# Kernel optimization log

Hardware: AMD Instinct MI355X
Metric: run time of the kernel (lower is better)

## Reference

```python
import jax, jax.numpy as jnp
import numpy as np

EPS = 1e-6


def _rmsnorm(x, weight, eps=EPS):
    # float32 compute, cast back to input dtype, then scale (matches torch module)
    xf = x.astype(jnp.float32)
    rms = jax.lax.rsqrt(jnp.mean(xf * xf, axis=-1, keepdims=True) + eps)
    return (xf * rms).astype(x.dtype) * weight


def _block_attn_res(V, pseudo_query, norm_weight):
    # V: [n, b, t, d]; pseudo_query, norm_weight: [d]
    K = _rmsnorm(V, norm_weight)                          # [n,b,t,d]
    d = pseudo_query.shape[-1]
    logits = jnp.einsum('d,nbtd->nbt', pseudo_query, K) / jnp.sqrt(jnp.float32(d))
    attn = jax.nn.softmax(logits, axis=0)                 # softmax over block axis n
    return jnp.einsum('nbt,nbtd->btd', attn, V)           # [b,t,d]


def setup_inputs() -> dict:
    key = jax.random.key(0)
    ks = jax.random.split(key, 4)
    N, B, T, D = 7, 2, 4096, 2048
    return {
        'blocks': jax.random.normal(ks[0], (N, B, T, D), dtype=jnp.float32),
        'partial_block': jax.random.normal(ks[1], (B, T, D), dtype=jnp.float32),
        'pseudo_query_attn': jax.random.normal(ks[2], (D,), dtype=jnp.float32),
        'pseudo_query_mlp': jax.random.normal(ks[3], (D,), dtype=jnp.float32),
        'norm_weight_attn': jnp.ones((D,), dtype=jnp.float32),
        'norm_weight_mlp': jnp.ones((D,), dtype=jnp.float32),
    }


def reference(blocks, partial_block, pseudo_query_attn, pseudo_query_mlp,
              norm_weight_attn, norm_weight_mlp):
    # V = stack(blocks + [partial_block], dim=0): [N+1, B, T, D]
    V = jnp.concatenate([blocks, partial_block[None]], axis=0)
    h_attn = _block_attn_res(V, pseudo_query_attn, norm_weight_attn)
    h_mlp = _block_attn_res(V, pseudo_query_mlp, norm_weight_mlp)
    return (h_attn, h_mlp)
```

## Files before the change

kernel.cpp:

```cpp
#include <hip/hip_runtime.h>

#define NB 8
#define DDIM 2048
#define THREADS 256
#define PER 8

typedef float f32x4 __attribute__((ext_vector_type(4)));

__device__ __forceinline__ float wave_sum64(float x) {
    int t;
    t = __builtin_amdgcn_update_dpp(0, __float_as_int(x), 0x111, 0xf, 0xf, false);
    x += __int_as_float(t);
    t = __builtin_amdgcn_update_dpp(0, __float_as_int(x), 0x112, 0xf, 0xf, false);
    x += __int_as_float(t);
    t = __builtin_amdgcn_update_dpp(0, __float_as_int(x), 0x114, 0xf, 0xf, false);
    x += __int_as_float(t);
    t = __builtin_amdgcn_update_dpp(0, __float_as_int(x), 0x118, 0xf, 0xf, false);
    x += __int_as_float(t);
    t = __builtin_amdgcn_update_dpp(0, __float_as_int(x), 0x142, 0xa, 0xf, false);
    x += __int_as_float(t);
    t = __builtin_amdgcn_update_dpp(0, __float_as_int(x), 0x143, 0xc, 0xf, false);
    x += __int_as_float(t);
    return x;
}

__global__ __launch_bounds__(THREADS, 4)
void block_attn_res_kernel(
    const float* __restrict__ blocks,
    const float* __restrict__ partial,
    const float* __restrict__ qa,
    const float* __restrict__ qm,
    const float* __restrict__ wa,
    const float* __restrict__ wm,
    float* __restrict__ out,
    int BT)
{
    const int row = blockIdx.x;
    const int tid = threadIdx.x;
    const int d0  = tid * PER;

    const size_t rowOff  = (size_t)row * DDIM + d0;
    const size_t nStride = (size_t)BT * DDIM;

    f32x4 qwa[2], qwm[2];
#pragma unroll
    for (int k = 0; k < 2; ++k) {
        const f32x4 q4a = *reinterpret_cast<const f32x4*>(qa + d0 + 4 * k);
        const f32x4 w4a = *reinterpret_cast<const f32x4*>(wa + d0 + 4 * k);
        const f32x4 q4m = *reinterpret_cast<const f32x4*>(qm + d0 + 4 * k);
        const f32x4 w4m = *reinterpret_cast<const f32x4*>(wm + d0 + 4 * k);
        qwa[k] = q4a * w4a;
        qwm[k] = q4m * w4m;
    }

    f32x4 v[NB][2];
    float ss[NB], da[NB], dm[NB];

#pragma unroll
    for (int n = 0; n < NB; ++n) {
        const float* src = (n < NB - 1) ? (blocks + (size_t)n * nStride + rowOff)
                                        : (partial + rowOff);
        v[n][0] = *reinterpret_cast<const f32x4*>(src);
        v[n][1] = *reinterpret_cast<const f32x4*>(src + 4);
        float s = 0.f, pa = 0.f, pm = 0.f;
#pragma unroll
        for (int k = 0; k < 2; ++k) {
#pragma unroll
            for (int j = 0; j < 4; ++j) {
                s  += v[n][k][j] * v[n][k][j];
                pa += qwa[k][j]  * v[n][k][j];
                pm += qwm[k][j]  * v[n][k][j];
            }
        }
        ss[n] = s; da[n] = pa; dm[n] = pm;
    }

#pragma unroll
    for (int n = 0; n < NB; ++n) {
        ss[n] = wave_sum64(ss[n]);
        da[n] = wave_sum64(da[n]);
        dm[n] = wave_sum64(dm[n]);
    }

    __shared__ float red[4 * 24];
    const int wave = tid >> 6;
    if ((tid & 63) == 63) {
#pragma unroll
        for (int n = 0; n < NB; ++n) {
            red[wave * 24 + n]      = ss[n];
            red[wave * 24 + 8 + n]  = da[n];
            red[wave * 24 + 16 + n] = dm[n];
        }
    }
    __syncthreads();

    float tot[24];
    {
        const f32x4* r4 = reinterpret_cast<const f32x4*>(red);
#pragma unroll
        for (int g = 0; g < 6; ++g) {
            f32x4 a = r4[g], b = r4[6 + g], c = r4[12 + g], d = r4[18 + g];
            f32x4 s4 = a + b + c + d;
            tot[4 * g + 0] = s4.x;
            tot[4 * g + 1] = s4.y;
            tot[4 * g + 2] = s4.z;
            tot[4 * g + 3] = s4.w;
        }
    }

    float aw[NB], mw[NB];
    {
        const float inv_sqrt_d = rsqrtf((float)DDIM);
        float lga[NB], lgm[NB];
#pragma unroll
        for (int n = 0; n < NB; ++n) {
            float rms = rsqrtf(tot[n] * (1.0f / DDIM) + 1e-6f);
            lga[n] = tot[8 + n]  * rms * inv_sqrt_d;
            lgm[n] = tot[16 + n] * rms * inv_sqrt_d;
        }
        float ma = lga[0], mm = lgm[0];
#pragma unroll
        for (int n = 1; n < NB; ++n) { ma = fmaxf(ma, lga[n]); mm = fmaxf(mm, lgm[n]); }
        float sa = 0.f, sm = 0.f;
#pragma unroll
        for (int n = 0; n < NB; ++n) {
            aw[n] = __expf(lga[n] - ma); sa += aw[n];
            mw[n] = __expf(lgm[n] - mm); sm += mw[n];
        }
        const float ra = 1.f / sa, rm = 1.f / sm;
#pragma unroll
        for (int n = 0; n < NB; ++n) { aw[n] *= ra; mw[n] *= rm; }
    }

    f32x4 oa[2], om[2];
#pragma unroll
    for (int k = 0; k < 2; ++k) {
        oa[k] = (f32x4)(0.f);
        om[k] = (f32x4)(0.f);
    }
#pragma unroll
    for (int n = 0; n < NB; ++n) {
#pragma unroll
        for (int k = 0; k < 2; ++k) {
            oa[k] += aw[n] * v[n][k];
            om[k] += mw[n] * v[n][k];
        }
    }

    float* outa = out + rowOff;
    float* outm = out + nStride + rowOff;
    *reinterpret_cast<f32x4*>(outa)     = oa[0];
    *reinterpret_cast<f32x4*>(outa + 4) = oa[1];
    *reinterpret_cast<f32x4*>(outm)     = om[0];
    *reinterpret_cast<f32x4*>(outm + 4) = om[1];
}

extern "C" void kernel_launch(void* const* d_in, const int* in_sizes, int n_in,
                              void* d_out, int out_size, void* d_ws, size_t ws_size,
                              hipStream_t stream)
{
    const float* blocks  = (const float*)d_in[0];
    const float* partial = (const float*)d_in[1];
    const float* qa      = (const float*)d_in[2];
    const float* qm      = (const float*)d_in[3];
    const float* wa      = (const float*)d_in[4];
    const float* wm      = (const float*)d_in[5];
    float* out = (float*)d_out;

    const int D  = in_sizes[2];
    const int BT = in_sizes[1] / D;

    dim3 grid(BT), block(THREADS);
    hipLaunchKernelGGL(block_attn_res_kernel, grid, block, 0, stream,
                       blocks, partial, qa, qm, wa, wm, out, BT);
}
```

Measured before the change: 133.4 us.

## Use persistent blocks with double-buffered row prefetch across rows

The kernel now launches a fixed grid of 512 blocks of 512 threads instead of one block per row. Each block loops over its strided rows and prefetches the next row's eight block vectors into registers while the current row is reduced and written. The goal is to hide global load latency and cut block launch overhead in this memory-bound kernel. The cost is extra registers for two row buffers, two shared-memory barriers per row, and a hardcoded assumption that the row count divides evenly by the grid size.

New measurement: 176.9 us. +32.6%, slower.

```diff
diff --git a/kernel.cpp b/kernel.cpp
--- a/kernel.cpp
+++ b/kernel.cpp
@@ -2,8 +2,9 @@
 
 #define NB 8
 #define DDIM 2048
-#define THREADS 256
-#define PER 8
+#define THREADS 512
+#define NBLK 512
+#define NWAVES (THREADS / 64)
 
 typedef float f32x4 __attribute__((ext_vector_type(4)));
 
@@ -24,6 +25,11 @@
     return x;
 }
 
+__device__ __forceinline__ void barrier_lgkm() {
+    asm volatile("s_waitcnt lgkmcnt(0)" ::: "memory");
+    __builtin_amdgcn_s_barrier();
+}
+
 __global__ __launch_bounds__(THREADS, 4)
 void block_attn_res_kernel(
     const float* __restrict__ blocks,
@@ -35,124 +41,120 @@
     float* __restrict__ out,
     int BT)
 {
-    const int row = blockIdx.x;
     const int tid = threadIdx.x;
-    const int d0  = tid * PER;
+    const int b   = blockIdx.x;
+    const int c   = tid * 4;
+    const size_t nStride = (size_t)BT * DDIM;
+    const int rpb = BT / NBLK;
 
-    const size_t rowOff  = (size_t)row * DDIM + d0;
-    const size_t nStride = (size_t)BT * DDIM;
+    __shared__ float red[2][NWAVES * 24];
+    __shared__ float totl[2][24];
 
-    f32x4 qwa[2], qwm[2];
+    const f32x4 qwa = *reinterpret_cast<const f32x4*>(qa + c) *
+                      *reinterpret_cast<const f32x4*>(wa + c);
+    const f32x4 qwm = *reinterpret_cast<const f32x4*>(qm + c) *
+                      *reinterpret_cast<const f32x4*>(wm + c);
+
+    f32x4 vA[NB], vB[NB];
+
+    auto rowbase = [&](int i) -> size_t {
+        return (size_t)(i * NBLK + b) * DDIM + c;
+    };
+    auto load_row = [&](f32x4* v, size_t rb) {
 #pragma unroll
-    for (int k = 0; k < 2; ++k) {
-        const f32x4 q4a = *reinterpret_cast<const f32x4*>(qa + d0 + 4 * k);
-        const f32x4 w4a = *reinterpret_cast<const f32x4*>(wa + d0 + 4 * k);
-        const f32x4 q4m = *reinterpret_cast<const f32x4*>(qm + d0 + 4 * k);
-        const f32x4 w4m = *reinterpret_cast<const f32x4*>(wm + d0 + 4 * k);
-        qwa[k] = q4a * w4a;
-        qwm[k] = q4m * w4m;
-    }
+        for (int n = 0; n < NB; ++n) {
+            const float* src = (n < NB - 1) ? (blocks + (size_t)n * nStride + rb)
+                                            : (partial + rb);
+            v[n] = *reinterpret_cast<const f32x4*>(src);
+        }
+    };
 
-    f32x4 v[NB][2];
-    float ss[NB], da[NB], dm[NB];
-
+    auto process = [&](const f32x4* v, float* redb, float* totb, size_t rb) {
+        float ss[NB], da[NB], dm[NB];
 #pragma unroll
-    for (int n = 0; n < NB; ++n) {
-        const float* src = (n < NB - 1) ? (blocks + (size_t)n * nStride + rowOff)
-                                        : (partial + rowOff);
-        v[n][0] = *reinterpret_cast<const f32x4*>(src);
-        v[n][1] = *reinterpret_cast<const f32x4*>(src + 4);
-        float s = 0.f, pa = 0.f, pm = 0.f;
-#pragma unroll
-        for (int k = 0; k < 2; ++k) {
+        for (int n = 0; n < NB; ++n) {
+            float s = 0.f, pa = 0.f, pm = 0.f;
 #pragma unroll
             for (int j = 0; j < 4; ++j) {
-                s  += v[n][k][j] * v[n][k][j];
-                pa += qwa[k][j]  * v[n][k][j];
-                pm += qwm[k][j]  * v[n][k][j];
+                s  += v[n][j] * v[n][j];
+                pa += qwa[j]  * v[n][j];
+                pm += qwm[j]  * v[n][j];
+            }
+            ss[n] = wave_sum64(s);
+            da[n] = wave_sum64(pa);
+            dm[n] = wave_sum64(pm);
+        }
+        const int wave = tid >> 6;
+        if ((tid & 63) == 63) {
+#pragma unroll
+            for (int n = 0; n < NB; ++n) {
+                redb[wave * 24 + n]      = ss[n];
+                redb[wave * 24 + 8 + n]  = da[n];
+                redb[wave * 24 + 16 + n] = dm[n];
             }
         }
-        ss[n] = s; da[n] = pa; dm[n] = pm;
-    }
+        barrier_lgkm();
+        if (tid < 24) {
+            float s = 0.f;
+#pragma unroll
+            for (int w = 0; w < NWAVES; ++w) s += redb[w * 24 + tid];
+            totb[tid] = s;
+        }
+        barrier_lgkm();
 
+        float t24[24];
+        {
+            const f32x4* t4 = reinterpret_cast<const f32x4*>(totb);
 #pragma unroll
-    for (int n = 0; n < NB; ++n) {
-        ss[n] = wave_sum64(ss[n]);
-        da[n] = wave_sum64(da[n]);
-        dm[n] = wave_sum64(dm[n]);
-    }
+            for (int g = 0; g < 6; ++g) {
+                f32x4 x = t4[g];
+                t24[4 * g + 0] = x.x; t24[4 * g + 1] = x.y;
+                t24[4 * g + 2] = x.z; t24[4 * g + 3] = x.w;
+            }
+        }
 
-    __shared__ float red[4 * 24];
-    const int wave = tid >> 6;
-    if ((tid & 63) == 63) {
+        float aw[NB], mw[NB];
+        {
+            const float inv_sqrt_d = rsqrtf((float)DDIM);
+            float lga[NB], lgm[NB];
+#pragma unroll
+            for (int n = 0; n < NB; ++n) {
+                float rms = rsqrtf(t24[n] * (1.0f / DDIM) + 1e-6f);
+                lga[n] = t24[8 + n]  * rms * inv_sqrt_d;
+                lgm[n] = t24[16 + n] * rms * inv_sqrt_d;
+            }
+            float ma = lga[0], mm = lgm[0];
+#pragma unroll
+            for (int n = 1; n < NB; ++n) { ma = fmaxf(ma, lga[n]); mm = fmaxf(mm, lgm[n]); }
+            float sa = 0.f, sm = 0.f;
+#pragma unroll
+            for (int n = 0; n < NB; ++n) {
+                aw[n] = __expf(lga[n] - ma); sa += aw[n];
+                mw[n] = __expf(lgm[n] - mm); sm += mw[n];
+            }
+            const float ra = 1.f / sa, rm = 1.f / sm;
+#pragma unroll
+            for (int n = 0; n < NB; ++n) { aw[n] *= ra; mw[n] *= rm; }
+        }
+
+        f32x4 oa = (f32x4)(0.f), om = (f32x4)(0.f);
 #pragma unroll
         for (int n = 0; n < NB; ++n) {
-            red[wave * 24 + n]      = ss[n];
-            red[wave * 24 + 8 + n]  = da[n];
-            red[wave * 24 + 16 + n] = dm[n];
+            oa += aw[n] * v[n];
+            om += mw[n] * v[n];
         }
+        *reinterpret_cast<f32x4*>(out + rb)           = oa;
+        *reinterpret_cast<f32x4*>(out + nStride + rb) = om;
+    };
+
+    load_row(vA, rowbase(0));
+#pragma unroll 1
+    for (int i = 0; i < rpb; i += 2) {
+        load_row(vB, rowbase(i + 1 < rpb ? i + 1 : rpb - 1));
+        process(vA, red[0], totl[0], rowbase(i));
+        load_row(vA, rowbase(i + 2 < rpb ? i + 2 : rpb - 1));
+        if (i + 1 < rpb) process(vB, red[1], totl[1], rowbase(i + 1));
     }
-    __syncthreads();
-
-    float tot[24];
-    {
-        const f32x4* r4 = reinterpret_cast<const f32x4*>(red);
-#pragma unroll
-        for (int g = 0; g < 6; ++g) {
-            f32x4 a = r4[g], b = r4[6 + g], c = r4[12 + g], d = r4[18 + g];
-            f32x4 s4 = a + b + c + d;
-            tot[4 * g + 0] = s4.x;
-            tot[4 * g + 1] = s4.y;
-            tot[4 * g + 2] = s4.z;
-            tot[4 * g + 3] = s4.w;
-        }
-    }
-
-    float aw[NB], mw[NB];
-    {
-        const float inv_sqrt_d = rsqrtf((float)DDIM);
-        float lga[NB], lgm[NB];
-#pragma unroll
-        for (int n = 0; n < NB; ++n) {
-            float rms = rsqrtf(tot[n] * (1.0f / DDIM) + 1e-6f);
-            lga[n] = tot[8 + n]  * rms * inv_sqrt_d;
-            lgm[n] = tot[16 + n] * rms * inv_sqrt_d;
-        }
-        float ma = lga[0], mm = lgm[0];
-#pragma unroll
-        for (int n = 1; n < NB; ++n) { ma = fmaxf(ma, lga[n]); mm = fmaxf(mm, lgm[n]); }
-        float sa = 0.f, sm = 0.f;
-#pragma unroll
-        for (int n = 0; n < NB; ++n) {
-            aw[n] = __expf(lga[n] - ma); sa += aw[n];
-            mw[n] = __expf(lgm[n] - mm); sm += mw[n];
-        }
-        const float ra = 1.f / sa, rm = 1.f / sm;
-#pragma unroll
-        for (int n = 0; n < NB; ++n) { aw[n] *= ra; mw[n] *= rm; }
-    }
-
-    f32x4 oa[2], om[2];
-#pragma unroll
-    for (int k = 0; k < 2; ++k) {
-        oa[k] = (f32x4)(0.f);
-        om[k] = (f32x4)(0.f);
-    }
-#pragma unroll
-    for (int n = 0; n < NB; ++n) {
-#pragma unroll
-        for (int k = 0; k < 2; ++k) {
-            oa[k] += aw[n] * v[n][k];
-            om[k] += mw[n] * v[n][k];
-        }
-    }
-
-    float* outa = out + rowOff;
-    float* outm = out + nStride + rowOff;
-    *reinterpret_cast<f32x4*>(outa)     = oa[0];
-    *reinterpret_cast<f32x4*>(outa + 4) = oa[1];
-    *reinterpret_cast<f32x4*>(outm)     = om[0];
-    *reinterpret_cast<f32x4*>(outm + 4) = om[1];
 }
 
 extern "C" void kernel_launch(void* const* d_in, const int* in_sizes, int n_in,
@@ -170,7 +172,7 @@
     const int D  = in_sizes[2];
     const int BT = in_sizes[1] / D;
 
-    dim3 grid(BT), block(THREADS);
+    dim3 grid(NBLK), block(THREADS);
     hipLaunchKernelGGL(block_attn_res_kernel, grid, block, 0, stream,
                        blocks, partial, qa, qm, wa, wm, out, BT);
 }
```
